# Kernel optimization log

Measured on AMD Instinct MI355X. Metric: run time of the kernel, lower is better.

The kernel has to match this reference:

```python
import jax, jax.numpy as jnp
import numpy as np

BETA = 1.0
B, N, D = 2048, 131072, 256

def setup_inputs() -> dict:
    key = jax.random.key(0)
    k1, k2 = jax.random.split(key)
    x = jax.random.normal(k1, (B, D), dtype=jnp.float32)
    stored = jax.random.normal(k2, (N, D), dtype=jnp.float32)
    return {"x": x, "stored": stored}

def reference(x, stored):
    # scores: [B, N] = beta * x @ stored^T
    scores = BETA * jnp.einsum('bd,nd->bn', x, stored)
    attn = jax.nn.softmax(scores, axis=-1)
    # retrieved patterns: [B, D]
    return jnp.einsum('bn,nd->bd', attn, stored)
```

## Files before the change

### kernel.cpp

```cpp
#include <hip/hip_runtime.h>
#include <hip/hip_bf16.h>
#include <math.h>

#define B_Q 2048
#define N_K 131072
#define D_DIM 256
#define NCHUNK 32
#define CHUNK_KEYS (N_K / NCHUNK)
#define KTILE 32
#define NITER (CHUNK_KEYS / KTILE)
#define NTILES (N_K / KTILE)
#define TILE_USHORTS 16384

typedef __attribute__((ext_vector_type(8))) _Float16 half8;
typedef __attribute__((ext_vector_type(8))) short bf16x8;
typedef __attribute__((ext_vector_type(2))) __fp16 fp16x2;
typedef __attribute__((ext_vector_type(4))) float f32x4;
typedef __attribute__((ext_vector_type(16))) float f32x16;

static __device__ __forceinline__ unsigned pkrtz(float a, float b) {
    fp16x2 h = __builtin_amdgcn_cvt_pkrtz(a, b);
    return __builtin_bit_cast(unsigned, h);
}
static __device__ __forceinline__ unsigned short f2bf(float f) {
    unsigned u = __builtin_bit_cast(unsigned, f);
    unsigned r = (u + 0x7fffu + ((u >> 16) & 1u)) >> 16;
    return (unsigned short)r;
}
static __device__ __forceinline__ unsigned cvt_pk_bf16(float lo, float hi) {
    unsigned d;
    asm("v_cvt_pk_bf16_f32 %0, %1, %2" : "=v"(d) : "v"(lo), "v"(hi));
    return d;
}

typedef const __attribute__((address_space(1))) unsigned int* gas_p;
typedef __attribute__((address_space(3))) unsigned int* las_p;
static __device__ __forceinline__ void gl_lds16(const void* g, void* l) {
    __builtin_amdgcn_global_load_lds((gas_p)g, (las_p)l, 16, 0, 0);
}

__global__ __launch_bounds__(512) void prepass(const float* __restrict__ stored,
                                               unsigned short* __restrict__ frag) {
    __shared__ float sh[32][270];
    const int tid = threadIdx.x;
    const int t = blockIdx.x;
    const float* src = stored + (size_t)t * 32 * 256;
#pragma unroll
    for (int i = 0; i < 8; ++i) {
        int gi = i * 512 + tid;
        int row = gi >> 7, c2 = (gi & 127) << 1;
        *(float2*)&sh[row][c2] = *(const float2*)(src + row * 256 + c2);
    }
    __syncthreads();
    unsigned short* out = frag + (size_t)t * TILE_USHORTS;
#pragma unroll
    for (int i = 0; i < 2; ++i) {
        int ck = i * 512 + tid;
        int l = ck & 63, s = ck >> 6;
        int key = l & 31, h = l >> 5;
        int d0 = s * 16 + h * 8;
        union { uint4 v; unsigned e[4]; } o;
#pragma unroll
        for (int j2 = 0; j2 < 4; ++j2) {
            float2 f = *(const float2*)&sh[key][d0 + j2 * 2];
            o.e[j2] = pkrtz(f.x, f.y);
        }
        *(uint4*)(out + ck * 8) = o.v;
    }
#pragma unroll
    for (int i = 0; i < 2; ++i) {
        int cv = i * 512 + tid;
        int l = cv & 63, blkv = cv >> 6;
        int dn = blkv >> 1, ks = blkv & 1;
        int colv = l & 31, h = l >> 5;
        int d = dn * 32 + colv;
        int k0 = ks * 16 + h * 8;
        union { uint4 v; unsigned e[4]; } o;
#pragma unroll
        for (int j2 = 0; j2 < 4; ++j2) {
            float v0 = sh[k0 + j2 * 2][d];
            float v1 = sh[k0 + j2 * 2 + 1][d];
            o.e[j2] = (unsigned)f2bf(v0) | ((unsigned)f2bf(v1) << 16);
        }
        *(uint4*)(out + 8192 + cv * 8) = o.v;
    }
}

__global__ __launch_bounds__(256, 2)
void hopfield_main(const float* __restrict__ x,
                   const unsigned short* __restrict__ frag,
                   float* __restrict__ partO,
                   float* __restrict__ partl) {
    __shared__ __align__(16) unsigned short Kb[2][8192];
    __shared__ __align__(16) unsigned short Vb[2][8192];

    const int tid = threadIdx.x;
    const int wave = tid >> 6, lane = tid & 63;
    const int col = lane & 31, hf = lane >> 5;
    const int blk = blockIdx.x;
    const int chunk = blk & 31, qb = blk >> 5;
    const int q0w = qb * 128 + wave * 32;
    const unsigned short* fbase = frag + (size_t)chunk * NITER * TILE_USHORTS;

    half8 xf[16];
    float ss = 0.f;
    {
        const float* xr = x + (size_t)(q0w + col) * 256 + hf * 8;
#pragma unroll
        for (int s = 0; s < 16; ++s) {
            f32x4 a = *(const f32x4*)(xr + s * 16);
            f32x4 b = *(const f32x4*)(xr + s * 16 + 4);
            union { half8 v; _Float16 e[8]; } h;
#pragma unroll
            for (int j = 0; j < 4; ++j) {
                h.e[j] = (_Float16)a[j]; h.e[4 + j] = (_Float16)b[j];
                ss += a[j] * a[j] + b[j] * b[j];
            }
            xf[s] = h.v;
        }
    }
    ss += __shfl_xor(ss, 32);
    const float M0 = 4.9f * sqrtf(ss);
    const float M0L = M0 * 1.44269504f;

    f32x16 O[8];
    const f32x16 z16 = {0.f,0.f,0.f,0.f,0.f,0.f,0.f,0.f,
                        0.f,0.f,0.f,0.f,0.f,0.f,0.f,0.f};
#pragma unroll
    for (int dn = 0; dn < 8; ++dn) O[dn] = z16;
    float lacc = 0.f;
    bf16x8 pa[2];
    pa[0] = (bf16x8){0,0,0,0,0,0,0,0};
    pa[1] = (bf16x8){0,0,0,0,0,0,0,0};

#pragma unroll
    for (int j = 0; j < 4; ++j) {
        int off = (wave * 4 + j) * 512 + lane * 8;
        gl_lds16(fbase + off, &Kb[0][off]);
        gl_lds16(fbase + 8192 + off, &Vb[0][off]);
    }

#pragma unroll 1
    for (int it = 0; it < NITER; ++it) {
        if (it) {
            const unsigned short* V = Vb[(it + 1) & 1];
            __builtin_amdgcn_s_setprio(1);
#pragma unroll
            for (int dn = 0; dn < 8; ++dn) {
                bf16x8 bv0 = *(const bf16x8*)(V + ((dn * 2 + 0) * 64 + lane) * 8);
                bf16x8 bv1 = *(const bf16x8*)(V + ((dn * 2 + 1) * 64 + lane) * 8);
                O[dn] = __builtin_amdgcn_mfma_f32_32x32x16_bf16(pa[0], bv0, O[dn], 0, 0, 0);
                O[dn] = __builtin_amdgcn_mfma_f32_32x32x16_bf16(pa[1], bv1, O[dn], 0, 0, 0);
            }
            __builtin_amdgcn_s_setprio(0);
        }
        __syncthreads();

        if (it + 1 < NITER) {
            const unsigned short* nbase = fbase + (size_t)(it + 1) * TILE_USHORTS;
#pragma unroll
            for (int j = 0; j < 4; ++j) {
                int off = (wave * 4 + j) * 512 + lane * 8;
                gl_lds16(nbase + off, &Kb[(it + 1) & 1][off]);
                gl_lds16(nbase + 8192 + off, &Vb[(it + 1) & 1][off]);
            }
        }

        const unsigned short* K = Kb[it & 1];
        f32x16 S = z16;
        __builtin_amdgcn_s_setprio(1);
#pragma unroll
        for (int s = 0; s < 16; ++s) {
            half8 af = *(const half8*)(K + (s * 64 + lane) * 8);
            S = __builtin_amdgcn_mfma_f32_32x32x16_f16(af, xf[s], S, 0, 0, 0);
        }
        __builtin_amdgcn_s_setprio(0);

        float p[16];
#pragma unroll
        for (int r = 0; r < 16; ++r)
            p[r] = __builtin_amdgcn_exp2f(fmaf(S[r], 1.44269504f, -M0L));
        float ps01 = (p[0] + p[1]) + (p[2] + p[3]);
        float ps23 = (p[4] + p[5]) + (p[6] + p[7]);
        float ps45 = (p[8] + p[9]) + (p[10] + p[11]);
        float ps67 = (p[12] + p[13]) + (p[14] + p[15]);
        lacc += (ps01 + ps23) + (ps45 + ps67);

        unsigned w0 = cvt_pk_bf16(p[0],  p[1]);
        unsigned w1 = cvt_pk_bf16(p[2],  p[3]);
        unsigned w2 = cvt_pk_bf16(p[4],  p[5]);
        unsigned w3 = cvt_pk_bf16(p[6],  p[7]);
        unsigned w4 = cvt_pk_bf16(p[8],  p[9]);
        unsigned w5 = cvt_pk_bf16(p[10], p[11]);
        unsigned w6 = cvt_pk_bf16(p[12], p[13]);
        unsigned w7 = cvt_pk_bf16(p[14], p[15]);
        asm volatile("v_permlane32_swap_b32 %0, %1" : "+v"(w0), "+v"(w2));
        asm volatile("v_permlane32_swap_b32 %0, %1" : "+v"(w1), "+v"(w3));
        asm volatile("v_permlane32_swap_b32 %0, %1" : "+v"(w4), "+v"(w6));
        asm volatile("v_permlane32_swap_b32 %0, %1" : "+v"(w5), "+v"(w7));
        union { bf16x8 v; unsigned u[4]; } A0, A1;
        A0.u[0] = w0; A0.u[1] = w1; A0.u[2] = w2; A0.u[3] = w3;
        A1.u[0] = w4; A1.u[1] = w5; A1.u[2] = w6; A1.u[3] = w7;
        pa[0] = A0.v; pa[1] = A1.v;
    }

    {
        const unsigned short* V = Vb[(NITER - 1) & 1];
#pragma unroll
        for (int dn = 0; dn < 8; ++dn) {
            bf16x8 bv0 = *(const bf16x8*)(V + ((dn * 2 + 0) * 64 + lane) * 8);
            bf16x8 bv1 = *(const bf16x8*)(V + ((dn * 2 + 1) * 64 + lane) * 8);
            O[dn] = __builtin_amdgcn_mfma_f32_32x32x16_bf16(pa[0], bv0, O[dn], 0, 0, 0);
            O[dn] = __builtin_amdgcn_mfma_f32_32x32x16_bf16(pa[1], bv1, O[dn], 0, 0, 0);
        }
    }

    lacc += __shfl_xor(lacc, 32);
    if (lane < 32)
        partl[(size_t)chunk * B_Q + q0w + lane] = lacc;

#pragma unroll
    for (int dn = 0; dn < 8; ++dn)
#pragma unroll
        for (int r = 0; r < 16; ++r) {
            int qrow = (r & 3) + 8 * (r >> 2) + 4 * hf;
            partO[((size_t)chunk * B_Q + q0w + qrow) * 256 + dn * 32 + col] = O[dn][r];
        }
}

__global__ void combine_kernel(const float* __restrict__ partO,
                               const float* __restrict__ partl,
                               float* __restrict__ out) {
    const int q = blockIdx.x;
    const int d = threadIdx.x;
    float L = 0.f;
#pragma unroll
    for (int c = 0; c < NCHUNK; ++c) L += partl[(size_t)c * B_Q + q];
    float acc = 0.f;
#pragma unroll
    for (int c = 0; c < NCHUNK; ++c)
        acc += partO[((size_t)c * B_Q + q) * 256 + d];
    out[(size_t)q * 256 + d] = acc / L;
}

extern "C" void kernel_launch(void* const* d_in, const int* in_sizes, int n_in,
                              void* d_out, int out_size, void* d_ws, size_t ws_size,
                              hipStream_t stream) {
    const float* x      = (const float*)d_in[0];
    const float* stored = (const float*)d_in[1];
    float* out = (float*)d_out;

    char* wsb = (char*)d_ws;
    unsigned short* frag = (unsigned short*)wsb;
    float* partO = (float*)(wsb + (size_t)134217728);
    float* partl = (float*)(wsb + (size_t)134217728 + 67108864);

    prepass<<<NTILES, 512, 0, stream>>>(stored, frag);
    hopfield_main<<<512, 256, 0, stream>>>(x, frag, partO, partl);
    combine_kernel<<<B_Q, 256, 0, stream>>>(partO, partl, out);
}
```

Measured before the change: 478.5 us.

## Fold log2e into K, seed S with offset, split PV MFMA into halves

Pre-scales the fp16 K fragments by log2(e) during conversion and seeds the score accumulator with the negative max offset, so each exponent is a bare exp2 with no FMA. The PV product now runs in the same iteration as its scores instead of one iteration late. It is split into two halves so the second half's exp/convert can overlap the first half's MFMAs. This drops the cross-iteration software pipeline, which may expose more latency between the QK MFMAs and the PV MFMAs. Scaling K by log2(e) before the fp16 cast also changes rounding slightly.

```diff
diff --git a/kernel.cpp b/kernel.cpp
--- a/kernel.cpp
+++ b/kernel.cpp
@@ -11,6 +11,7 @@
 #define NITER (CHUNK_KEYS / KTILE)
 #define NTILES (N_K / KTILE)
 #define TILE_USHORTS 16384
+#define LOG2E 1.44269504f
 
 typedef __attribute__((ext_vector_type(8))) _Float16 half8;
 typedef __attribute__((ext_vector_type(8))) short bf16x8;
@@ -63,7 +64,7 @@
 #pragma unroll
         for (int j2 = 0; j2 < 4; ++j2) {
             float2 f = *(const float2*)&sh[key][d0 + j2 * 2];
-            o.e[j2] = pkrtz(f.x, f.y);
+            o.e[j2] = pkrtz(f.x * LOG2E, f.y * LOG2E);
         }
         *(uint4*)(out + ck * 8) = o.v;
     }
@@ -120,8 +121,7 @@
         }
     }
     ss += __shfl_xor(ss, 32);
-    const float M0 = 4.9f * sqrtf(ss);
-    const float M0L = M0 * 1.44269504f;
+    const float negM0L = -(4.9f * sqrtf(ss) * LOG2E);
 
     f32x16 O[8];
     const f32x16 z16 = {0.f,0.f,0.f,0.f,0.f,0.f,0.f,0.f,
@@ -129,9 +129,6 @@
 #pragma unroll
     for (int dn = 0; dn < 8; ++dn) O[dn] = z16;
     float lacc = 0.f;
-    bf16x8 pa[2];
-    pa[0] = (bf16x8){0,0,0,0,0,0,0,0};
-    pa[1] = (bf16x8){0,0,0,0,0,0,0,0};
 
 #pragma unroll
     for (int j = 0; j < 4; ++j) {
@@ -142,18 +139,6 @@
 
 #pragma unroll 1
     for (int it = 0; it < NITER; ++it) {
-        if (it) {
-            const unsigned short* V = Vb[(it + 1) & 1];
-            __builtin_amdgcn_s_setprio(1);
-#pragma unroll
-            for (int dn = 0; dn < 8; ++dn) {
-                bf16x8 bv0 = *(const bf16x8*)(V + ((dn * 2 + 0) * 64 + lane) * 8);
-                bf16x8 bv1 = *(const bf16x8*)(V + ((dn * 2 + 1) * 64 + lane) * 8);
-                O[dn] = __builtin_amdgcn_mfma_f32_32x32x16_bf16(pa[0], bv0, O[dn], 0, 0, 0);
-                O[dn] = __builtin_amdgcn_mfma_f32_32x32x16_bf16(pa[1], bv1, O[dn], 0, 0, 0);
-            }
-            __builtin_amdgcn_s_setprio(0);
-        }
         __syncthreads();
 
         if (it + 1 < NITER) {
@@ -167,7 +152,11 @@
         }
 
         const unsigned short* K = Kb[it & 1];
-        f32x16 S = z16;
+        const unsigned short* V = Vb[it & 1];
+
+        f32x16 S;
+#pragma unroll
+        for (int r = 0; r < 16; ++r) S[r] = negM0L;
         __builtin_amdgcn_s_setprio(1);
 #pragma unroll
         for (int s = 0; s < 16; ++s) {
@@ -176,43 +165,49 @@
         }
         __builtin_amdgcn_s_setprio(0);
 
-        float p[16];
-#pragma unroll
-        for (int r = 0; r < 16; ++r)
-            p[r] = __builtin_amdgcn_exp2f(fmaf(S[r], 1.44269504f, -M0L));
-        float ps01 = (p[0] + p[1]) + (p[2] + p[3]);
-        float ps23 = (p[4] + p[5]) + (p[6] + p[7]);
-        float ps45 = (p[8] + p[9]) + (p[10] + p[11]);
-        float ps67 = (p[12] + p[13]) + (p[14] + p[15]);
-        lacc += (ps01 + ps23) + (ps45 + ps67);
-
-        unsigned w0 = cvt_pk_bf16(p[0],  p[1]);
-        unsigned w1 = cvt_pk_bf16(p[2],  p[3]);
-        unsigned w2 = cvt_pk_bf16(p[4],  p[5]);
-        unsigned w3 = cvt_pk_bf16(p[6],  p[7]);
-        unsigned w4 = cvt_pk_bf16(p[8],  p[9]);
-        unsigned w5 = cvt_pk_bf16(p[10], p[11]);
-        unsigned w6 = cvt_pk_bf16(p[12], p[13]);
-        unsigned w7 = cvt_pk_bf16(p[14], p[15]);
+        float p0[8];
+#pragma unroll
+        for (int r = 0; r < 8; ++r) p0[r] = __builtin_amdgcn_exp2f(S[r]);
+        lacc += ((p0[0] + p0[1]) + (p0[2] + p0[3])) + ((p0[4] + p0[5]) + (p0[6] + p0[7]));
+        unsigned w0 = cvt_pk_bf16(p0[0], p0[1]);
+        unsigned w1 = cvt_pk_bf16(p0[2], p0[3]);
+        unsigned w2 = cvt_pk_bf16(p0[4], p0[5]);
+        unsigned w3 = cvt_pk_bf16(p0[6], p0[7]);
         asm volatile("v_permlane32_swap_b32 %0, %1" : "+v"(w0), "+v"(w2));
         asm volatile("v_permlane32_swap_b32 %0, %1" : "+v"(w1), "+v"(w3));
+        union { bf16x8 v; unsigned u[4]; } A0;
+        A0.u[0] = w0; A0.u[1] = w1; A0.u[2] = w2; A0.u[3] = w3;
+        bf16x8 pa0 = A0.v;
+
+        __builtin_amdgcn_s_setprio(1);
+#pragma unroll
+        for (int dn = 0; dn < 8; ++dn) {
+            bf16x8 bv0 = *(const bf16x8*)(V + ((dn * 2 + 0) * 64 + lane) * 8);
+            O[dn] = __builtin_amdgcn_mfma_f32_32x32x16_bf16(pa0, bv0, O[dn], 0, 0, 0);
+        }
+        __builtin_amdgcn_s_setprio(0);
+
+        float p1[8];
+#pragma unroll
+        for (int r = 0; r < 8; ++r) p1[r] = __builtin_amdgcn_exp2f(S[8 + r]);
+        lacc += ((p1[0] + p1[1]) + (p1[2] + p1[3])) + ((p1[4] + p1[5]) + (p1[6] + p1[7]));
+        unsigned w4 = cvt_pk_bf16(p1[0], p1[1]);
+        unsigned w5 = cvt_pk_bf16(p1[2], p1[3]);
+        unsigned w6 = cvt_pk_bf16(p1[4], p1[5]);
+        unsigned w7 = cvt_pk_bf16(p1[6], p1[7]);
         asm volatile("v_permlane32_swap_b32 %0, %1" : "+v"(w4), "+v"(w6));
         asm volatile("v_permlane32_swap_b32 %0, %1" : "+v"(w5), "+v"(w7));
-        union { bf16x8 v; unsigned u[4]; } A0, A1;
-        A0.u[0] = w0; A0.u[1] = w1; A0.u[2] = w2; A0.u[3] = w3;
+        union { bf16x8 v; unsigned u[4]; } A1;
         A1.u[0] = w4; A1.u[1] = w5; A1.u[2] = w6; A1.u[3] = w7;
-        pa[0] = A0.v; pa[1] = A1.v;
-    }
-
-    {
-        const unsigned short* V = Vb[(NITER - 1) & 1];
+        bf16x8 pa1 = A1.v;
+
+        __builtin_amdgcn_s_setprio(1);
 #pragma unroll
         for (int dn = 0; dn < 8; ++dn) {
-            bf16x8 bv0 = *(const bf16x8*)(V + ((dn * 2 + 0) * 64 + lane) * 8);
             bf16x8 bv1 = *(const bf16x8*)(V + ((dn * 2 + 1) * 64 + lane) * 8);
-            O[dn] = __builtin_amdgcn_mfma_f32_32x32x16_bf16(pa[0], bv0, O[dn], 0, 0, 0);
-            O[dn] = __builtin_amdgcn_mfma_f32_32x32x16_bf16(pa[1], bv1, O[dn], 0, 0, 0);
-        }
+            O[dn] = __builtin_amdgcn_mfma_f32_32x32x16_bf16(pa1, bv1, O[dn], 0, 0, 0);
+        }
+        __builtin_amdgcn_s_setprio(0);
     }
 
     lacc += __shfl_xor(lacc, 32);
```

Measured after the change: 476.8 us. No clear change (-0.3%).
